# Kernel optimization log

Measured on AMD Instinct MI355X. Metric: run time of the kernel, lower is better.

The kernel has to match this reference:

```python
import jax, jax.numpy as jnp
import numpy as np


def setup_inputs() -> dict:
    key = jax.random.key(0)
    k1, k2, k3, k4, k5 = jax.random.split(key, 5)
    NNZ = 1_600_000
    N, IN, OUT = 8192, 4096, 4096
    vals = jax.random.normal(k1, (NNZ,), dtype=jnp.float32)
    rows = jax.random.randint(k2, (NNZ,), 0, N, dtype=jnp.int32)
    cols = jax.random.randint(k3, (NNZ,), 0, IN, dtype=jnp.int32)
    # kaiming_uniform-ish init scale for weight, uniform bias
    bound_w = jnp.sqrt(1.0 / IN)
    weight = jax.random.uniform(k4, (OUT, IN), dtype=jnp.float32, minval=-bound_w, maxval=bound_w)
    bias = jax.random.uniform(k5, (OUT,), dtype=jnp.float32, minval=-bound_w, maxval=bound_w)
    return {"vals": vals, "rows": rows, "cols": cols, "weight": weight, "bias": bias, "n_rows": N}


def reference(vals, rows, cols, weight, bias, n_rows):
    """Sparse COO [n_rows, in_features] @ weight.T + bias (torch.sparse.addmm).

    Densify via scatter-add (COO semantics: duplicate indices accumulate),
    then a single dense GEMM which dominates the cost.
    """
    in_features = weight.shape[1]
    dense = jnp.zeros((n_rows, in_features), dtype=vals.dtype).at[rows, cols].add(vals)
    return dense @ weight.T + bias  # [n_rows, out_features]
```

## Files before the change

### kernel.cpp

```cpp
#include <hip/hip_runtime.h>

typedef __attribute__((ext_vector_type(8)))  __bf16 bf16x8;
typedef __attribute__((ext_vector_type(16))) float  f32x16;
typedef __attribute__((ext_vector_type(4)))  float  f32x4;
typedef __attribute__((ext_vector_type(8)))  unsigned short u16x8;

#define TM 128
#define TN 128
#define BK 64

__device__ inline unsigned short f2bf(float f) {
    unsigned int u = __float_as_uint(f);
    u += 0x7FFFu + ((u >> 16) & 1u);
    return (unsigned short)(u >> 16);
}

__global__ __launch_bounds__(256) void scatter_bf16(
        const float* __restrict__ vals,
        const int* __restrict__ rows,
        const int* __restrict__ cols,
        unsigned short* __restrict__ Ab,
        int nnz, int in_f) {
    int i = blockIdx.x * blockDim.x + threadIdx.x;
    if (i >= nnz) return;
    float v = vals[i];
    size_t idx = (size_t)rows[i] * in_f + cols[i];
    unsigned int* word = (unsigned int*)(Ab + (idx & ~(size_t)1));
    unsigned int sh = (unsigned int)(idx & 1) * 16u;
    unsigned int old = *word, assumed;
    do {
        assumed = old;
        unsigned int cur = (assumed >> sh) & 0xFFFFu;
        float f = __uint_as_float(cur << 16) + v;
        unsigned int nb = f2bf(f);
        unsigned int repl = (assumed & ~(0xFFFFu << sh)) | (nb << sh);
        old = atomicCAS(word, assumed, repl);
    } while (old != assumed);
}

__global__ __launch_bounds__(256) void cvt_kernel(
        const float* __restrict__ src,
        unsigned short* __restrict__ dst,
        long n) {
    long i = ((long)blockIdx.x * blockDim.x + threadIdx.x) * 8;
    if (i + 8 <= n) {
        f32x4 a = *(const f32x4*)(src + i);
        f32x4 b = *(const f32x4*)(src + i + 4);
        u16x8 o;
        o[0] = f2bf(a[0]); o[1] = f2bf(a[1]); o[2] = f2bf(a[2]); o[3] = f2bf(a[3]);
        o[4] = f2bf(b[0]); o[5] = f2bf(b[1]); o[6] = f2bf(b[2]); o[7] = f2bf(b[3]);
        *(u16x8*)(dst + i) = o;
    }
}

__global__ __launch_bounds__(256) void gemm_bt_bias(
    const unsigned short* __restrict__ A,
    const unsigned short* __restrict__ B,
    const float* __restrict__ bias,
    float* __restrict__ C,
    int M, int N, int K)
{
    __shared__ unsigned short sA[TM * BK];
    __shared__ unsigned short sB[TN * BK];

    const int tid  = threadIdx.x;
    const int lane = tid & 63;
    const int wave = tid >> 6;
    const int wm = (wave >> 1) * 64;
    const int wn = (wave & 1) * 64;
    const int bm = blockIdx.y * TM;
    const int bn = blockIdx.x * TN;

    const int m32 = lane & 31;
    const int h   = lane >> 5;
    const int sw  = m32 & 7;

    f32x16 acc[2][2];
    #pragma unroll
    for (int t = 0; t < 2; ++t)
        #pragma unroll
        for (int u = 0; u < 2; ++u)
            #pragma unroll
            for (int r = 0; r < 16; ++r)
                acc[t][u][r] = 0.f;

    for (int k0 = 0; k0 < K; k0 += BK) {
        #pragma unroll
        for (int i = 0; i < 4; ++i) {
            int c   = tid + i * 256;
            int row = c >> 3;
            int kc  = (c & 7) ^ (row & 7);
            const unsigned short* ga = A + (size_t)(bm + row) * K + k0 + kc * 8;
            const unsigned short* gb = B + (size_t)(bn + row) * K + k0 + kc * 8;
            unsigned short* la = sA + (size_t)(wave * 64 + i * 256) * 8;
            unsigned short* lb = sB + (size_t)(wave * 64 + i * 256) * 8;
            __builtin_amdgcn_global_load_lds(
                (const __attribute__((address_space(1))) void*)ga,
                (__attribute__((address_space(3))) void*)la, 16, 0, 0);
            __builtin_amdgcn_global_load_lds(
                (const __attribute__((address_space(1))) void*)gb,
                (__attribute__((address_space(3))) void*)lb, 16, 0, 0);
        }
        __syncthreads();

        #pragma unroll
        for (int kc = 0; kc < 4; ++kc) {
            const int cs = (kc * 2 + h) ^ sw;
            bf16x8 a0 = *(const bf16x8*)(sA + (wm      + m32) * BK + cs * 8);
            bf16x8 a1 = *(const bf16x8*)(sA + (wm + 32 + m32) * BK + cs * 8);
            bf16x8 b0 = *(const bf16x8*)(sB + (wn      + m32) * BK + cs * 8);
            bf16x8 b1 = *(const bf16x8*)(sB + (wn + 32 + m32) * BK + cs * 8);
            acc[0][0] = __builtin_amdgcn_mfma_f32_32x32x16_bf16(a0, b0, acc[0][0], 0, 0, 0);
            acc[0][1] = __builtin_amdgcn_mfma_f32_32x32x16_bf16(a0, b1, acc[0][1], 0, 0, 0);
            acc[1][0] = __builtin_amdgcn_mfma_f32_32x32x16_bf16(a1, b0, acc[1][0], 0, 0, 0);
            acc[1][1] = __builtin_amdgcn_mfma_f32_32x32x16_bf16(a1, b1, acc[1][1], 0, 0, 0);
        }
        __syncthreads();
    }

    #pragma unroll
    for (int u = 0; u < 2; ++u) {
        int col = bn + wn + u * 32 + m32;
        float bv = bias[col];
        #pragma unroll
        for (int t = 0; t < 2; ++t) {
            int rbase = bm + wm + t * 32 + 4 * h;
            #pragma unroll
            for (int r = 0; r < 16; ++r) {
                int row = rbase + (r & 3) + 8 * (r >> 2);
                __builtin_nontemporal_store(acc[t][u][r] + bv,
                                            &C[(size_t)row * N + col]);
            }
        }
    }
}

extern "C" void kernel_launch(void* const* d_in, const int* in_sizes, int n_in,
                              void* d_out, int out_size, void* d_ws, size_t ws_size,
                              hipStream_t stream) {
    const float* vals   = (const float*)d_in[0];
    const int*   rows   = (const int*)d_in[1];
    const int*   cols   = (const int*)d_in[2];
    const float* weight = (const float*)d_in[3];
    const float* bias   = (const float*)d_in[4];

    const int NNZ = in_sizes[0];
    const int OUT = in_sizes[4];
    const int IN  = in_sizes[3] / OUT;
    const int M   = out_size / OUT;

    unsigned short* Ab = (unsigned short*)d_ws;
    size_t abBytes = (size_t)M * IN * sizeof(unsigned short);
    unsigned short* Wb = (unsigned short*)((char*)d_ws + abBytes);

    hipMemsetAsync(Ab, 0, abBytes, stream);

    scatter_bf16<<<(NNZ + 255) / 256, 256, 0, stream>>>(vals, rows, cols, Ab, NNZ, IN);

    {
        long nW = (long)OUT * IN;
        cvt_kernel<<<(int)((nW / 8 + 255) / 256), 256, 0, stream>>>(weight, Wb, nW);
    }

    dim3 grid(OUT / TN, M / TM);
    gemm_bt_bias<<<grid, 256, 0, stream>>>(Ab, Wb, bias, (float*)d_out, M, OUT, IN);
}
```

Baseline: 553.4 us.

## Rewrite GEMM with 256x256 tiles, double-buffered LDS pipeline and XCD-aware block remap

Replaces the 128x128 single-buffered GEMM with a 512-thread, 256x256 block tile that double-buffers 32-wide K slabs in LDS. Global-to-LDS loads for future slabs are issued between MFMA phases, with explicit waitcnt, barriers and priority raises. It also switches to 16x16x32 MFMA fragments and remaps block IDs across groups of 8 for locality across chiplets. The goal is to hide load latency and raise arithmetic intensity, at the cost of heavier LDS use, more register pressure and fragile hand-placed synchronization.

```diff
diff --git a/kernel.cpp b/kernel.cpp
--- a/kernel.cpp
+++ b/kernel.cpp
@@ -1,13 +1,8 @@
 #include <hip/hip_runtime.h>
 
 typedef __attribute__((ext_vector_type(8)))  __bf16 bf16x8;
-typedef __attribute__((ext_vector_type(16))) float  f32x16;
 typedef __attribute__((ext_vector_type(4)))  float  f32x4;
 typedef __attribute__((ext_vector_type(8)))  unsigned short u16x8;
-
-#define TM 128
-#define TN 128
-#define BK 64
 
 __device__ inline unsigned short f2bf(float f) {
     unsigned int u = __float_as_uint(f);
@@ -53,83 +48,156 @@
     }
 }
 
-__global__ __launch_bounds__(256) void gemm_bt_bias(
+
+__device__ __forceinline__ bf16x8 read_frag(const unsigned short* slab, int row, int g) {
+    return *(const bf16x8*)(slab + row * 32 + ((g ^ (row & 3)) << 3));
+}
+
+__device__ __forceinline__ void stage_slab(const unsigned short* __restrict__ G,
+                                           int grow0, int K, int kelem,
+                                           unsigned short* slab, int tid) {
+    const int lane = tid & 63, wv = tid >> 6;
+    #pragma unroll
+    for (int j = 0; j < 2; ++j) {
+        int u = wv * 128 + j * 64 + lane;
+        int row = u >> 2, slot = u & 3;
+        const unsigned short* g = G + (size_t)(grow0 + row) * K
+                                    + (kelem + ((slot ^ (row & 3)) << 3));
+        unsigned short* l = slab + (wv * 128 + j * 64) * 8;
+        __builtin_amdgcn_global_load_lds(
+            (const __attribute__((address_space(1))) void*)g,
+            (__attribute__((address_space(3))) void*)l, 16, 0, 0);
+    }
+}
+
+__global__ __launch_bounds__(512, 2) void gemm_bt_bias(
     const unsigned short* __restrict__ A,
     const unsigned short* __restrict__ B,
     const float* __restrict__ bias,
     float* __restrict__ C,
     int M, int N, int K)
 {
-    __shared__ unsigned short sA[TM * BK];
-    __shared__ unsigned short sB[TN * BK];
+    __shared__ unsigned short sA[2][2][8192];
+    __shared__ unsigned short sB[2][2][8192];
 
     const int tid  = threadIdx.x;
     const int lane = tid & 63;
     const int wave = tid >> 6;
-    const int wm = (wave >> 1) * 64;
-    const int wn = (wave & 1) * 64;
-    const int bm = blockIdx.y * TM;
-    const int bn = blockIdx.x * TN;
-
-    const int m32 = lane & 31;
-    const int h   = lane >> 5;
-    const int sw  = m32 & 7;
-
-    f32x16 acc[2][2];
+    const int wm = (wave >> 2) * 128;
+    const int wn = (wave & 3) * 64;
+    const int r15 = lane & 15;
+    const int g   = lane >> 4;
+
+    const int nbx = gridDim.x;
+    const int nwg = gridDim.x * gridDim.y;
+    int flat = blockIdx.y * gridDim.x + blockIdx.x;
+    int rid = (nwg & 7) ? flat : ((flat & 7) * (nwg >> 3) + (flat >> 3));
+    const int bm = (rid / nbx) * 256;
+    const int bn = (rid % nbx) * 256;
+
+    f32x4 acc[8][4];
     #pragma unroll
-    for (int t = 0; t < 2; ++t)
-        #pragma unroll
-        for (int u = 0; u < 2; ++u)
+    for (int i = 0; i < 8; ++i)
+        #pragma unroll
+        for (int jg = 0; jg < 4; ++jg)
             #pragma unroll
-            for (int r = 0; r < 16; ++r)
-                acc[t][u][r] = 0.f;
-
-    for (int k0 = 0; k0 < K; k0 += BK) {
-        #pragma unroll
-        for (int i = 0; i < 4; ++i) {
-            int c   = tid + i * 256;
-            int row = c >> 3;
-            int kc  = (c & 7) ^ (row & 7);
-            const unsigned short* ga = A + (size_t)(bm + row) * K + k0 + kc * 8;
-            const unsigned short* gb = B + (size_t)(bn + row) * K + k0 + kc * 8;
-            unsigned short* la = sA + (size_t)(wave * 64 + i * 256) * 8;
-            unsigned short* lb = sB + (size_t)(wave * 64 + i * 256) * 8;
-            __builtin_amdgcn_global_load_lds(
-                (const __attribute__((address_space(1))) void*)ga,
-                (__attribute__((address_space(3))) void*)la, 16, 0, 0);
-            __builtin_amdgcn_global_load_lds(
-                (const __attribute__((address_space(1))) void*)gb,
-                (__attribute__((address_space(3))) void*)lb, 16, 0, 0);
-        }
-        __syncthreads();
-
-        #pragma unroll
-        for (int kc = 0; kc < 4; ++kc) {
-            const int cs = (kc * 2 + h) ^ sw;
-            bf16x8 a0 = *(const bf16x8*)(sA + (wm      + m32) * BK + cs * 8);
-            bf16x8 a1 = *(const bf16x8*)(sA + (wm + 32 + m32) * BK + cs * 8);
-            bf16x8 b0 = *(const bf16x8*)(sB + (wn      + m32) * BK + cs * 8);
-            bf16x8 b1 = *(const bf16x8*)(sB + (wn + 32 + m32) * BK + cs * 8);
-            acc[0][0] = __builtin_amdgcn_mfma_f32_32x32x16_bf16(a0, b0, acc[0][0], 0, 0, 0);
-            acc[0][1] = __builtin_amdgcn_mfma_f32_32x32x16_bf16(a0, b1, acc[0][1], 0, 0, 0);
-            acc[1][0] = __builtin_amdgcn_mfma_f32_32x32x16_bf16(a1, b0, acc[1][0], 0, 0, 0);
-            acc[1][1] = __builtin_amdgcn_mfma_f32_32x32x16_bf16(a1, b1, acc[1][1], 0, 0, 0);
-        }
-        __syncthreads();
+            for (int r = 0; r < 4; ++r) acc[i][jg][r] = 0.f;
+
+    stage_slab(A, bm, K, 0,       &sA[0][0][0], tid);
+    stage_slab(B, bn, K, 0,       &sB[0][0][0], tid);
+    stage_slab(A, bm, K, 32,      &sA[0][1][0], tid);
+    stage_slab(B, bn, K, 32,      &sB[0][1][0], tid);
+    stage_slab(A, bm, K, 64,      &sA[1][0][0], tid);
+    stage_slab(B, bn, K, 64,      &sB[1][0][0], tid);
+    asm volatile("s_waitcnt vmcnt(8)" ::: "memory");
+    __builtin_amdgcn_s_barrier();
+
+    const int nt = K >> 6;
+    for (int t = 0; t < nt; ++t) {
+        const int cur = t & 1, nxt = cur ^ 1;
+        const int t1k = ((t + 1 < nt) ? t + 1 : 0) << 6;
+        const int t2k = ((t + 2 < nt) ? t + 2 : 0) << 6;
+        const unsigned short* sAc0 = &sA[cur][0][0];
+        const unsigned short* sAc1 = &sA[cur][1][0];
+        const unsigned short* sBc0 = &sB[cur][0][0];
+        const unsigned short* sBc1 = &sB[cur][1][0];
+
+        bf16x8 a[8], b[2];
+
+        #pragma unroll
+        for (int i = 0; i < 8; ++i) a[i] = read_frag(sAc0, wm + i * 16 + r15, g);
+        b[0] = read_frag(sBc0, wn + r15, g);
+        b[1] = read_frag(sBc0, wn + 16 + r15, g);
+        stage_slab(A, bm, K, t1k + 32, &sA[nxt][1][0], tid);
+        __builtin_amdgcn_s_barrier();
+        asm volatile("s_waitcnt lgkmcnt(0)" ::: "memory");
+        __builtin_amdgcn_s_setprio(1);
+        #pragma unroll
+        for (int i = 0; i < 8; ++i) {
+            acc[i][0] = __builtin_amdgcn_mfma_f32_16x16x32_bf16(a[i], b[0], acc[i][0], 0, 0, 0);
+            acc[i][1] = __builtin_amdgcn_mfma_f32_16x16x32_bf16(a[i], b[1], acc[i][1], 0, 0, 0);
+        }
+        __builtin_amdgcn_s_setprio(0);
+        __builtin_amdgcn_s_barrier();
+
+        b[0] = read_frag(sBc0, wn + 32 + r15, g);
+        b[1] = read_frag(sBc0, wn + 48 + r15, g);
+        stage_slab(B, bn, K, t1k + 32, &sB[nxt][1][0], tid);
+        __builtin_amdgcn_s_barrier();
+        asm volatile("s_waitcnt lgkmcnt(0)" ::: "memory");
+        __builtin_amdgcn_s_setprio(1);
+        #pragma unroll
+        for (int i = 0; i < 8; ++i) {
+            acc[i][2] = __builtin_amdgcn_mfma_f32_16x16x32_bf16(a[i], b[0], acc[i][2], 0, 0, 0);
+            acc[i][3] = __builtin_amdgcn_mfma_f32_16x16x32_bf16(a[i], b[1], acc[i][3], 0, 0, 0);
+        }
+        __builtin_amdgcn_s_setprio(0);
+        asm volatile("s_waitcnt vmcnt(8)" ::: "memory");
+        __builtin_amdgcn_s_barrier();
+
+        #pragma unroll
+        for (int i = 0; i < 8; ++i) a[i] = read_frag(sAc1, wm + i * 16 + r15, g);
+        b[0] = read_frag(sBc1, wn + r15, g);
+        b[1] = read_frag(sBc1, wn + 16 + r15, g);
+        stage_slab(A, bm, K, t2k, &sA[cur][0][0], tid);
+        __builtin_amdgcn_s_barrier();
+        asm volatile("s_waitcnt lgkmcnt(0)" ::: "memory");
+        __builtin_amdgcn_s_setprio(1);
+        #pragma unroll
+        for (int i = 0; i < 8; ++i) {
+            acc[i][0] = __builtin_amdgcn_mfma_f32_16x16x32_bf16(a[i], b[0], acc[i][0], 0, 0, 0);
+            acc[i][1] = __builtin_amdgcn_mfma_f32_16x16x32_bf16(a[i], b[1], acc[i][1], 0, 0, 0);
+        }
+        __builtin_amdgcn_s_setprio(0);
+        __builtin_amdgcn_s_barrier();
+
+        b[0] = read_frag(sBc1, wn + 32 + r15, g);
+        b[1] = read_frag(sBc1, wn + 48 + r15, g);
+        stage_slab(B, bn, K, t2k, &sB[cur][0][0], tid);
+        __builtin_amdgcn_s_barrier();
+        asm volatile("s_waitcnt lgkmcnt(0)" ::: "memory");
+        __builtin_amdgcn_s_setprio(1);
+        #pragma unroll
+        for (int i = 0; i < 8; ++i) {
+            acc[i][2] = __builtin_amdgcn_mfma_f32_16x16x32_bf16(a[i], b[0], acc[i][2], 0, 0, 0);
+            acc[i][3] = __builtin_amdgcn_mfma_f32_16x16x32_bf16(a[i], b[1], acc[i][3], 0, 0, 0);
+        }
+        __builtin_amdgcn_s_setprio(0);
+        asm volatile("s_waitcnt vmcnt(8)" ::: "memory");
+        __builtin_amdgcn_s_barrier();
     }
 
     #pragma unroll
-    for (int u = 0; u < 2; ++u) {
-        int col = bn + wn + u * 32 + m32;
+    for (int jg = 0; jg < 4; ++jg) {
+        int col = bn + wn + jg * 16 + r15;
         float bv = bias[col];
         #pragma unroll
-        for (int t = 0; t < 2; ++t) {
-            int rbase = bm + wm + t * 32 + 4 * h;
+        for (int i = 0; i < 8; ++i) {
+            int rbase = bm + wm + i * 16 + g * 4;
             #pragma unroll
-            for (int r = 0; r < 16; ++r) {
-                int row = rbase + (r & 3) + 8 * (r >> 2);
-                __builtin_nontemporal_store(acc[t][u][r] + bv,
-                                            &C[(size_t)row * N + col]);
+            for (int r = 0; r < 4; ++r) {
+                __builtin_nontemporal_store(acc[i][jg][r] + bv,
+                                            &C[(size_t)(rbase + r) * N + col]);
             }
         }
     }
@@ -162,6 +230,6 @@
         cvt_kernel<<<(int)((nW / 8 + 255) / 256), 256, 0, stream>>>(weight, Wb, nW);
     }
 
-    dim3 grid(OUT / TN, M / TM);
-    gemm_bt_bias<<<grid, 256, 0, stream>>>(Ab, Wb, bias, (float*)d_out, M, OUT, IN);
-}
+    dim3 grid(OUT / 256, M / 256);
+    gemm_bt_bias<<<grid, 512, 0, stream>>>(Ab, Wb, bias, (float*)d_out, M, OUT, IN);
+}
```

Result: faster. 535.8 us (-3.2%).
